# Performance work log

Measured on AMD Instinct MI355X. Metric: run time of the kernel, lower is better.

The kernel has to match this reference:

```python
import jax, jax.numpy as jnp
import numpy as np

B, L, D, N_LAYERS = 128, 256, 512, 6
NEG = -9e15  # -9000000000000000.0 in the torch source


def _pair_coef(a1, L, D):
    # Faithful reduction of the torch repeat_interleave(dim=2) construction:
    # first half of a_input satisfies a_input[b, i, j, m] = h[b, i, (j*D + m)//L],
    # so sum_m a_input[...,m]*a1[m] = h[b,i] . c[j] with
    # c[j, f] = sum_{m : (j*D+m)//L == f} a1[m].
    j = jnp.arange(L)[:, None]
    m = jnp.arange(D)[None, :]
    idx = (j * D + m) // L  # [L, D], values in [0, D-1]
    c = jnp.zeros((L, D), a1.dtype)
    c = c.at[jnp.arange(L)[:, None], idx].add(jnp.broadcast_to(a1[None, :], (L, D)))
    return c


def gat_layer(x, adj, W, a):
    # h = x @ W; e[b,i,j] = relu(a_input[b,i,j,:] @ a)  (relu overwrites leakyrelu in source)
    h = x @ W  # [B, L, D]
    d = W.shape[1]
    a1, a2 = a[:d, 0], a[d:, 0]
    c = _pair_coef(a1, h.shape[1], d)  # [L, D]
    e = jax.nn.relu(jnp.einsum('bif,jf->bij', h, c) + (h @ a2)[:, None, :])
    att = jnp.where(adj > 0, e, NEG)
    att = jax.nn.softmax(att, axis=2)  # dropout is identity in eval
    h_prime = jnp.einsum('bij,bjd->bid', att, h)
    return jax.nn.elu(h_prime)  # concat=True branch


def position_weight(x, left_len, aspect_len, text_len):
    j = jnp.arange(x.shape[1])[None, :].astype(jnp.float32)  # [1, L]
    l = left_len[:, None].astype(jnp.float32)
    r = (left_len + aspect_len - 1)[:, None].astype(jnp.float32)
    tl = text_len[:, None].astype(jnp.float32)
    ctx = (text_len - aspect_len)[:, None].astype(jnp.float32)
    w = jnp.where(j < l, 1.0 - (l - j) / ctx,
        jnp.where(j <= r, 0.0,
        jnp.where(j < tl, 1.0 - (j - r) / ctx, 0.0)))
    return w[..., None].astype(x.dtype) * x


def aspect_mask(x, left_len, aspect_len):
    j = jnp.arange(x.shape[1])[None, :]
    l = left_len[:, None]
    r = (left_len + aspect_len - 1)[:, None]
    m = ((j >= l) & (j <= r)).astype(x.dtype)
    return m[..., None] * x


def setup_inputs() -> dict:
    key = jax.random.key(0)
    ks = jax.random.split(key, 6)
    x = jax.random.normal(ks[0], (B, L, D), jnp.float32)
    adj = jax.random.randint(ks[1], (B, L, L), 0, 2, jnp.int32)
    adj = adj.at[:, jnp.arange(L), jnp.arange(L)].set(1)  # self loops
    left_len = jax.random.randint(ks[2], (B,), 0, 20, jnp.int32)
    aspect_len = jax.random.randint(ks[3], (B,), 1, 6, jnp.int32)
    text_len = jnp.full((B,), L, jnp.int32)
    W_stack = jax.random.normal(ks[4], (N_LAYERS, D, D), jnp.float32) * (1.414 / np.sqrt(D))
    a_stack = jax.random.normal(ks[5], (N_LAYERS, 2 * D, 1), jnp.float32) * 0.05
    return {"x": x, "W_stack": W_stack, "a_stack": a_stack, "adj": adj,
            "left_len": left_len, "aspect_len": aspect_len, "text_len": text_len}


def reference(x, W_stack, a_stack, adj, left_len, aspect_len, text_len):
    text_out = x
    xp = position_weight(text_out, left_len, aspect_len, text_len)
    h1 = jax.nn.relu(gat_layer(xp, adj, W_stack[0], a_stack[0]))
    h1 = position_weight(h1, left_len, aspect_len, text_len)
    x_graph = jnp.zeros_like(h1)
    for i in range(1, N_LAYERS):
        x_graph = x_graph + jax.nn.relu(gat_layer(h1, adj, W_stack[i], a_stack[i]))
    x_graph = 0.2 * x_graph
    graph_mask = aspect_mask(x_graph, left_len, aspect_len)
    # hop == 1 attention pooling
    alpha_mat = jnp.einsum('bld,bmd->blm', graph_mask, text_out)  # [B, L, L]
    alpha = jax.nn.softmax(alpha_mat.sum(axis=1, keepdims=True), axis=2)  # [B, 1, L]
    a1 = jnp.einsum('blm,bmd->bld', alpha, text_out)[:, 0, :]  # [B, D]
    return a1
```

## Files before the change

### kernel.cpp

```cpp
#include <hip/hip_runtime.h>

#define NB 128
#define NLQ 256
#define ND 512
#define NLAYERS 6
#define DD (ND*ND)
#define MN (1024*ND)
#define HTB 131072

typedef _Float16 f16x8 __attribute__((ext_vector_type(8)));
typedef __fp16 fp16x2 __attribute__((ext_vector_type(2)));
typedef _Float16 f16x4v __attribute__((ext_vector_type(4)));
typedef float f32x4 __attribute__((ext_vector_type(4)));
typedef unsigned int u32x2 __attribute__((ext_vector_type(2)));
typedef unsigned int u32x4 __attribute__((ext_vector_type(4)));
typedef unsigned short ushort_t;

#define GLOAD16(gp, lp) __builtin_amdgcn_global_load_lds( \
    (const __attribute__((address_space(1))) void*)(gp), \
    (__attribute__((address_space(3))) void*)(lp), 16, 0, 0)

__device__ __forceinline__ float wave_max(float v){
  #pragma unroll
  for(int off=32; off; off>>=1) v = fmaxf(v, __shfl_xor(v, off));
  return v;
}
__device__ __forceinline__ float wave_sum(float v){
  #pragma unroll
  for(int off=32; off; off>>=1) v += __shfl_xor(v, off);
  return v;
}
__device__ __forceinline__ unsigned int pk16(float a, float b){
  fp16x2 h = __builtin_amdgcn_cvt_pkrtz(a, b);
  return __builtin_bit_cast(unsigned int, h);
}

__global__ __launch_bounds__(256) void k_scal(const float* __restrict__ a_stack,
                                              float* __restrict__ scal){
  int layer = blockIdx.x;
  const float* a = a_stack + (size_t)layer*2*ND;
  int t = threadIdx.x;
  float v0 = a[t];
  float v1 = a[256 + t];
  v0 = wave_sum(v0); v1 = wave_sum(v1);
  __shared__ float s0[4], s1[4];
  int wave = t>>6, lane = t&63;
  if(lane==0){ s0[wave]=v0; s1[wave]=v1; }
  __syncthreads();
  if(t==0){
    scal[layer*2+0] = s0[0]+s0[1]+s0[2]+s0[3];
    scal[layer*2+1] = s1[0]+s1[1]+s1[2]+s1[3];
  }
}

__global__ __launch_bounds__(256) void k_wa2(const float* __restrict__ Wst,
                                             const float* __restrict__ ast,
                                             float* __restrict__ v){
  int l  = blockIdx.x >> 7;
  int rg = blockIdx.x & 127;
  int i  = rg*4 + (threadIdx.x>>6);
  int lane = threadIdx.x & 63;
  const float4* wr = (const float4*)(Wst + (size_t)(l+1)*DD + (size_t)i*ND);
  const float4* ar = (const float4*)(ast + (size_t)(l+1)*2*ND + ND);
  float4 w0=wr[lane], w1=wr[lane+64], a0=ar[lane], a1=ar[lane+64];
  float d = w0.x*a0.x + w0.y*a0.y + w0.z*a0.z + w0.w*a0.w
          + w1.x*a1.x + w1.y*a1.y + w1.z*a1.z + w1.w*a1.w;
  d = wave_sum(d);
  if(lane==0) v[l*ND + i] = d;
}

__global__ __launch_bounds__(256) void k_wcvt(const float* __restrict__ Wsrc,
                                              ushort_t* __restrict__ Ho){
  __shared__ float CT[64][65];
  int bid = blockIdx.x;
  int l  = bid >> 6;
  int kt = (bid >> 3) & 7, nt = bid & 7;
  const float* Wl = Wsrc + (size_t)l*DD;
  int t = threadIdx.x;
  int r = t >> 2, c4 = (t&3)*16;
  #pragma unroll
  for(int u=0;u<4;u++){
    float4 vv = *(const float4*)(Wl + (size_t)(kt*64+r)*ND + nt*64 + c4 + u*4);
    CT[r][c4+u*4+0]=vv.x; CT[r][c4+u*4+1]=vv.y;
    CT[r][c4+u*4+2]=vv.z; CT[r][c4+u*4+3]=vv.w;
  }
  __syncthreads();
  int n = t >> 2, kc = t & 3;
  unsigned int o[8];
  #pragma unroll
  for(int j=0;j<8;j++)
    o[j] = pk16(CT[kc*16 + 2*j][n], CT[kc*16 + 2*j + 1][n]);
  ushort_t* dh = Ho + (size_t)l*DD + (size_t)(nt*64+n)*ND + kt*64 + kc*16;
  *(u32x4*)(dh)     = (u32x4){o[0],o[1],o[2],o[3]};
  *(u32x4*)(dh + 8) = (u32x4){o[4],o[5],o[6],o[7]};
}

#define ROWB2 144
template<int MODE>
__device__ __forceinline__ void gemm_tile(const float* __restrict__ A,
                                          const ushort_t* __restrict__ Wth,
                                          float* __restrict__ C,
                                          unsigned int* __restrict__ hP,
                                          ushort_t* __restrict__ Pbuf,
                                          float* __restrict__ tp4,
                                          const float* __restrict__ a2,
                                          const float* __restrict__ scal,
                                          const int* __restrict__ left,
                                          const int* __restrict__ asp,
                                          const int* __restrict__ tl,
                                          int mtile, int ntile, unsigned char* lds){
  unsigned char* Ah = lds;
  unsigned char* Bh = lds + 128*ROWB2;

  int t = threadIdx.x;
  int m0 = mtile*128, n0 = ntile*128;
  int lane = t & 63, wid = t >> 6;
  int wr = wid >> 2, wcq = wid & 3;
  int lrow = lane & 15, kb = lane >> 4;

  f32x4 acc[4][2];
  #pragma unroll
  for(int mi=0;mi<4;mi++)
    #pragma unroll
    for(int ni=0;ni<2;ni++)
      acc[mi][ni] = (f32x4){0.f,0.f,0.f,0.f};

  int a_row = t >> 4;
  int a_sl  = t & 15;
  int w_n   = t >> 3;
  int w_sl  = t & 7;

  float wgt_[4] = {1.f,1.f,1.f,1.f};
  if(MODE == 1){
    int b = mtile >> 1;
    float lf=(float)left[b], aspf=(float)asp[b], tlf=(float)tl[b];
    float rr=lf+aspf-1.f, ctx=tlf-aspf;
    #pragma unroll
    for(int u=0;u<4;u++){
      float jf = (float)((mtile&1)*128 + a_row + u*32);
      float w;
      if(jf < lf)       w = 1.f-(lf-jf)/ctx;
      else if(jf <= rr) w = 0.f;
      else if(jf < tlf) w = 1.f-(jf-rr)/ctx;
      else              w = 0.f;
      wgt_[u] = w;
    }
  }

  float4 pa[4];
  u32x4 pwh[2];

  #pragma unroll
  for(int u=0;u<4;u++)
    pa[u] = *(const float4*)(A + (size_t)(m0 + a_row + u*32)*ND + a_sl*4);
  #pragma unroll
  for(int u=0;u<2;u++)
    pwh[u] = *(const u32x4*)(Wth + (size_t)(n0 + w_n + u*64)*ND + w_sl*8);

  for(int k0=0; k0<ND; k0+=64){
    #pragma unroll
    for(int u=0;u<4;u++){
      unsigned int c0 = pk16(pa[u].x*wgt_[u], pa[u].y*wgt_[u]);
      unsigned int c1 = pk16(pa[u].z*wgt_[u], pa[u].w*wgt_[u]);
      *(u32x2*)(Ah + (a_row + u*32)*ROWB2 + a_sl*8) = (u32x2){c0, c1};
    }
    #pragma unroll
    for(int u=0;u<2;u++)
      *(u32x4*)(Bh + (w_n + u*64)*ROWB2 + w_sl*16) = pwh[u];
    __syncthreads();

    if(k0 + 64 < ND){
      int kn = k0 + 64;
      #pragma unroll
      for(int u=0;u<4;u++)
        pa[u] = *(const float4*)(A + (size_t)(m0 + a_row + u*32)*ND + kn + a_sl*4);
      #pragma unroll
      for(int u=0;u<2;u++)
        pwh[u] = *(const u32x4*)(Wth + (size_t)(n0 + w_n + u*64)*ND + kn + w_sl*8);
    }

    #pragma unroll
    for(int ks=0; ks<2; ks++){
      f16x8 ah[4], bh[2];
      #pragma unroll
      for(int mi=0;mi<4;mi++)
        ah[mi] = *(const f16x8*)(Ah + (wr*64 + mi*16 + lrow)*ROWB2 + ks*64 + kb*16);
      #pragma unroll
      for(int ni=0;ni<2;ni++)
        bh[ni] = *(const f16x8*)(Bh + (wcq*32 + ni*16 + lrow)*ROWB2 + ks*64 + kb*16);
      #pragma unroll
      for(int mi=0;mi<4;mi++)
        #pragma unroll
        for(int ni=0;ni<2;ni++)
          acc[mi][ni] = __builtin_amdgcn_mfma_f32_16x16x32_f16(ah[mi], bh[ni], acc[mi][ni], 0,0,0);
    }
    __syncthreads();
  }

  int rg = lane >> 4;
  int cc = lane & 15;
  if(MODE == 0){
    #pragma unroll
    for(int mi=0;mi<4;mi++)
      #pragma unroll
      for(int ni=0;ni<2;ni++){
        int col = n0 + wcq*32 + ni*16 + cc;
        #pragma unroll
        for(int q=0;q<4;q++){
          int row = m0 + wr*64 + mi*16 + rg*4 + q;
          C[(size_t)row*ND + col] = acc[mi][ni][q];
        }
      }
  } else {
    float S0 = scal[0], S1 = scal[1];
    float* CT = (float*)lds;
    int b = m0 >> 8;
    int ibase = m0 & 255;
    int tr   = t >> 2;
    int tch  = t & 3;
    float tpsum = 0.f;
    #pragma unroll
    for(int p=0;p<2;p++){
      if((wcq>>1) == p){
        #pragma unroll
        for(int mi=0;mi<4;mi++)
          #pragma unroll
          for(int ni=0;ni<2;ni++)
            #pragma unroll
            for(int q=0;q<4;q++)
              CT[((wcq&1)*32 + ni*16 + cc)*130 + wr*64 + mi*16 + rg*4 + q] = acc[mi][ni][q];
      }
      __syncthreads();
      int lcol = t >> 6;
      int lrow2 = (t & 63)*2;
      #pragma unroll
      for(int u=0;u<8;u++){
        int c = lcol + u*8;
        float2 v2 = *(float2*)&CT[c*130 + lrow2];
        size_t uidx = ((size_t)b*HTB + (size_t)(n0 + p*64 + c)*256 + ibase + lrow2) >> 1;
        hP[uidx] = pk16(v2.x, v2.y);
      }
      {
        int cpr = t & 31;
        int rq  = t >> 5;
        #pragma unroll
        for(int rr2=0; rr2<8; rr2++){
          int row = rq*8 + rr2;
          float pval = S0*CT[(2*cpr)*130 + row] + S1*CT[(2*cpr+1)*130 + row];
          int ig = ibase + row;
          _Float16 ph = (_Float16)pval;
          size_t addr = (size_t)b*262144 + (size_t)(ig>>5)*32768
                      + (size_t)(ig&31)*256 + (n0>>1) + p*32 + cpr;
          Pbuf[addr] = __builtin_bit_cast(unsigned short, ph);
        }
      }
      #pragma unroll
      for(int cc2=0; cc2<16; cc2++){
        int c = tch*16 + cc2;
        tpsum = fmaf(CT[c*130 + tr], a2[n0 + p*64 + c], tpsum);
      }
      __syncthreads();
    }
    tpsum += __shfl_xor(tpsum, 1);
    tpsum += __shfl_xor(tpsum, 2);
    if(tch == 0) tp4[(n0>>7)*32768 + m0 + tr] = tpsum;
  }
}

__global__ __launch_bounds__(512) void k_gemm_t(const float* __restrict__ A,
                                                const ushort_t* __restrict__ Wth,
                                                unsigned int* __restrict__ hP,
                                                ushort_t* __restrict__ Pbuf,
                                                float* __restrict__ tp4,
                                                const float* __restrict__ a2,
                                                const float* __restrict__ scal,
                                                const int* __restrict__ left,
                                                const int* __restrict__ asp,
                                                const int* __restrict__ tl){
  __shared__ unsigned char lds[2*128*ROWB2];
  int bid = blockIdx.x;
  int ntile = (bid >> 3) & 3;
  int mtile = (bid & 7) | ((bid >> 5) << 3);
  gemm_tile<1>(A, Wth, nullptr, hP, Pbuf, tp4, a2, scal, left, asp, tl,
               mtile, ntile, lds);
}

__global__ __launch_bounds__(512) void k_gemm_b(const float* __restrict__ Abase, long aStride,
                                                const ushort_t* __restrict__ Wth,
                                                float* __restrict__ Cbase){
  __shared__ unsigned char lds[2*128*ROWB2];
  int l  = blockIdx.x >> 5;
  int tb = blockIdx.x & 31;
  gemm_tile<0>(Abase + (size_t)l*aStride, Wth + (size_t)l*DD,
               Cbase + (size_t)l*MN, nullptr, nullptr, nullptr,
               nullptr, nullptr, nullptr, nullptr, nullptr, tb>>2, tb&3, lds);
}

__global__ __launch_bounds__(256) void k_attn0(
    const ushort_t* __restrict__ hTH,
    const int* __restrict__ adj,
    const float* __restrict__ tpart,
    const int* __restrict__ left, const int* __restrict__ asp, const int* __restrict__ tl,
    float* __restrict__ PA){
  __shared__ unsigned char attH[32*512];
  __shared__ unsigned char BsH[16384];

  int bid = blockIdx.x;
  int b  = bid & 127;
  int ic = bid >> 7;
  int i0 = ic*32;
  int tid = threadIdx.x;
  int lane = tid & 63, w = tid >> 6;
  const ushort_t* HH = hTH + (size_t)b*HTB;
  const ushort_t* Pt = (const ushort_t*)PA + (size_t)b*262144 + (size_t)ic*32768;

  float t0v=0.f, t1v=0.f, t2v=0.f, t3v=0.f;
  #pragma unroll
  for(int nt=0; nt<4; nt++){
    float4 tv = ((const float4*)(tpart + nt*32768 + b*256))[lane];
    t0v += tv.x; t1v += tv.y; t2v += tv.z; t3v += tv.w;
  }

  for(int rr=0; rr<8; rr++){
    int il = w*8 + rr;
    int i  = i0 + il;
    f16x4v pv = *(const f16x4v*)(Pt + il*256 + lane*4);
    int4 av = ((const int4*)(adj + ((size_t)b*NLQ + i)*NLQ))[lane];
    float e0 = fmaxf((float)pv[0] + t0v, 0.f);
    float e1 = fmaxf((float)pv[1] + t1v, 0.f);
    float e2 = fmaxf((float)pv[2] + t2v, 0.f);
    float e3 = fmaxf((float)pv[3] + t3v, 0.f);
    float m = -3.0e38f;
    if(av.x>0) m = e0;
    if(av.y>0) m = fmaxf(m, e1);
    if(av.z>0) m = fmaxf(m, e2);
    if(av.w>0) m = fmaxf(m, e3);
    m = wave_max(m);
    float p0 = (av.x>0) ? __expf(e0-m) : 0.f;
    float p1 = (av.y>0) ? __expf(e1-m) : 0.f;
    float p2 = (av.z>0) ? __expf(e2-m) : 0.f;
    float p3 = (av.w>0) ? __expf(e3-m) : 0.f;
    float s = wave_sum(p0+p1+p2+p3);
    float inv = 1.f/s;
    unsigned int w0 = pk16(p0*inv, p1*inv);
    unsigned int w1 = pk16(p2*inv, p3*inv);
    int off = il*512 + ((lane*8) ^ ((il&7)<<4));
    *(u32x2*)(attH + off) = (u32x2){w0,w1};
  }

  int wm = w >> 1, wn = w & 1;
  int lrow = lane & 15, kb = lane >> 4;
  int rg = lane >> 4, cc = lane & 15;
  float lf=(float)left[b], aspf=(float)asp[b], tlf=(float)tl[b];
  float rrv=lf+aspf-1.f, ctx=tlf-aspf;
  int arow = wm*16 + lrow;
  int aswz = (arow&7)<<4;

  for(int dp=0; dp<2; dp++){
    int d0 = dp*256;
    f32x4 acc[8];
    #pragma unroll
    for(int ni=0;ni<8;ni++) acc[ni] = (f32x4){0.f,0.f,0.f,0.f};
    for(int ks=0; ks<8; ks++){
      int j0 = ks*32;
      __syncthreads();
      #pragma unroll
      for(int u=0;u<4;u++){
        int chunk = (u*4 + w)*64 + lane;
        int row = chunk >> 2, sl = chunk & 3;
        GLOAD16(HH + (size_t)(d0+row)*256 + j0 + sl*8, BsH + (u*4+w)*1024);
      }
      __syncthreads();
      int aoff = arow*512 + ((j0*2 + kb*16) ^ aswz);
      f16x8 ah = *(const f16x8*)(attH + aoff);
      #pragma unroll
      for(int ni=0; ni<8; ni++){
        f16x8 bh = *(const f16x8*)(BsH + (wn*128 + ni*16 + lrow)*64 + kb*16);
        acc[ni] = __builtin_amdgcn_mfma_f32_16x16x32_f16(ah, bh, acc[ni], 0,0,0);
      }
    }
    #pragma unroll
    for(int q=0;q<4;q++){
      int row = i0 + wm*16 + rg*4 + q;
      float fi = (float)row;
      float wgt;
      if(fi < lf)        wgt = 1.f-(lf-fi)/ctx;
      else if(fi <= rrv) wgt = 0.f;
      else if(fi < tlf)  wgt = 1.f-(fi-rrv)/ctx;
      else               wgt = 0.f;
      #pragma unroll
      for(int ni=0;ni<8;ni++){
        int col = d0 + wn*128 + ni*16 + cc;
        PA[((size_t)b*NLQ + row)*ND + col] = wgt*fmaxf(acc[ni][q], 0.f);
      }
    }
  }
}

__global__ __launch_bounds__(256) void k_tv(const float* __restrict__ h1,
                                            const float* __restrict__ v,
                                            float* __restrict__ T){
  int row  = blockIdx.x*4 + (threadIdx.x>>6);
  int lane = threadIdx.x & 63;
  const float4* hr = (const float4*)(h1 + (size_t)row*ND);
  float4 h0 = hr[lane], h1v = hr[lane+64];
  float s0,s1,s2,s3,s4;
  #define DOTV(SL, L) { \
    const float4* vr = (const float4*)(v + (L)*ND); \
    float4 v0 = vr[lane], v1 = vr[lane+64]; \
    float dd = h0.x*v0.x+h0.y*v0.y+h0.z*v0.z+h0.w*v0.w \
             + h1v.x*v1.x+h1v.y*v1.y+h1v.z*v1.z+h1v.w*v1.w; \
    SL = wave_sum(dd); }
  DOTV(s0,0) DOTV(s1,1) DOTV(s2,2) DOTV(s3,3) DOTV(s4,4)
  #undef DOTV
  if(lane==0){
    T[0*32768 + row]=s0; T[1*32768 + row]=s1; T[2*32768 + row]=s2;
    T[3*32768 + row]=s3; T[4*32768 + row]=s4;
  }
}

__global__ __launch_bounds__(256) void k_rows(const float* __restrict__ h1,
                                              const int* __restrict__ left, const int* __restrict__ asp,
                                              float* __restrict__ R){
  int b = blockIdx.x;
  int nk = asp[b], l0 = left[b];
  const float4* src = (const float4*)(h1 + (size_t)b*NLQ*ND);
  float4* dst = (float4*)(R + (size_t)b*8*ND);
  #pragma unroll
  for(int u=0; u<4; u++){
    int f4 = threadIdx.x + u*256;
    int k = f4 >> 7, c = f4 & 127;
    float4 val = (k<nk) ? src[(size_t)(l0+k)*128 + c] : (float4){0.f,0.f,0.f,0.f};
    dst[f4] = val;
  }
}

__global__ __launch_bounds__(256) void k_att5(const float* __restrict__ h1,
    const float* __restrict__ Hasp, const float* __restrict__ T,
    const int* __restrict__ adj, const float* __restrict__ scal,
    const int* __restrict__ left, const int* __restrict__ asp,
    float* __restrict__ y){
  __shared__ float att[5][260];
  int b  = blockIdx.x & 127;
  int l  = blockIdx.x >> 7;
  int tid = threadIdx.x, lane = tid&63, w = tid>>6;
  int nk = asp[b], l0 = left[b];
  float S0 = scal[2*(l+1)], S1 = scal[2*(l+1)+1];

  for(int k = w; k < 5; k += 4){
    if(k < nk){
      const float2* hrow = (const float2*)(Hasp + (size_t)l*MN + (size_t)(b*8+k)*ND);
      const int* arow = adj + ((size_t)b*NLQ + (l0+k))*NLQ;
      const float* Tl = T + l*32768 + b*256;
      float e[4]; int av[4];
      float m = -3.0e38f;
      #pragma unroll
      for(int q=0;q<4;q++){
        int j = lane + 64*q;
        float2 hp = hrow[j];
        av[q] = arow[j];
        e[q] = fmaxf(S0*hp.x + S1*hp.y + Tl[j], 0.f);
        if(av[q] > 0) m = fmaxf(m, e[q]);
      }
      m = wave_max(m);
      float pp[4]; float s = 0.f;
      #pragma unroll
      for(int q=0;q<4;q++){
        pp[q] = (av[q] > 0) ? __expf(e[q]-m) : 0.f;
        s += pp[q];
      }
      s = wave_sum(s);
      float inv = 1.f/s;
      #pragma unroll
      for(int q=0;q<4;q++) att[k][lane+64*q] = pp[q]*inv;
    } else {
      #pragma unroll
      for(int q=0;q<4;q++) att[k][lane+64*q] = 0.f;
    }
  }
  __syncthreads();

  int d = tid;
  const float* hb = h1 + (size_t)b*NLQ*ND;
  float ax[5] = {0,0,0,0,0}, ay[5] = {0,0,0,0,0};
  for(int jj=0; jj<NLQ; jj++){
    float hx = hb[(size_t)jj*ND + d];
    float hy = hb[(size_t)jj*ND + 256 + d];
    #pragma unroll
    for(int k=0;k<5;k++){
      float a = att[k][jj];
      ax[k] += a*hx;
      ay[k] += a*hy;
    }
  }
  float* yb = y + (size_t)l*MN + (size_t)b*8*ND;
  #pragma unroll
  for(int k=0;k<5;k++){
    yb[(size_t)k*ND + d]       = ax[k];
    yb[(size_t)k*ND + 256 + d] = ay[k];
  }
  #pragma unroll
  for(int u=0;u<6;u++) yb[5*ND + u*256 + tid] = 0.f;
}

__global__ __launch_bounds__(256) void k_g(const float* __restrict__ hp,
    const int* __restrict__ asp, float* __restrict__ g){
  int b = blockIdx.x, d = threadIdx.x;
  int nk = asp[b];
  float gx=0.f, gy=0.f;
  for(int l=0;l<5;l++){
    for(int k=0;k<nk;k++){
      const float* r = hp + (size_t)l*MN + (size_t)(b*8+k)*ND;
      gx += fmaxf(r[d], 0.f);
      gy += fmaxf(r[d+256], 0.f);
    }
  }
  g[b*ND + d]       = 0.2f*gx;
  g[b*ND + 256 + d] = 0.2f*gy;
}

__global__ __launch_bounds__(256) void k_dot(const float* __restrict__ x,
    const float* __restrict__ g, float* __restrict__ s){
  int row  = blockIdx.x*4 + (threadIdx.x>>6);
  int b    = row >> 8;
  int lane = threadIdx.x & 63;
  const float4* xr = (const float4*)(x + (size_t)row*ND);
  const float4* gr = (const float4*)(g + (size_t)b*ND);
  float4 x0=xr[lane], x1=xr[lane+64], g0=gr[lane], g1=gr[lane+64];
  float d = x0.x*g0.x + x0.y*g0.y + x0.z*g0.z + x0.w*g0.w
          + x1.x*g1.x + x1.y*g1.y + x1.z*g1.z + x1.w*g1.w;
  d = wave_sum(d);
  if(lane==0) s[row] = d;
}

__global__ __launch_bounds__(256) void k_out(const float* __restrict__ x,
    const float* __restrict__ s, float* __restrict__ out){
  int b  = blockIdx.x >> 2;
  int ch = blockIdx.x & 3;
  int tid = threadIdx.x, lane = tid&63, w = tid>>6;
  __shared__ float red[4];
  __shared__ float alpha[NLQ];
  __shared__ float part[128];
  float sv = s[b*NLQ + tid];
  float m = wave_max(sv);
  if(lane==0) red[w] = m;
  __syncthreads();
  m = fmaxf(fmaxf(red[0],red[1]), fmaxf(red[2],red[3]));
  float p = __expf(sv - m);
  float su = wave_sum(p);
  __syncthreads();
  if(lane==0) red[w] = su;
  __syncthreads();
  su = red[0]+red[1]+red[2]+red[3];
  alpha[tid] = p/su;
  __syncthreads();
  int d = ch*128 + (tid & 127);
  int half = tid >> 7;
  const float* xb = x + (size_t)b*NLQ*ND;
  float acc = 0.f;
  for(int mm = half*128; mm < half*128 + 128; mm++)
    acc += alpha[mm] * xb[(size_t)mm*ND + d];
  if(half) part[tid & 127] = acc;
  __syncthreads();
  if(!half) out[(size_t)b*ND + d] = acc + part[tid & 127];
}

extern "C" void kernel_launch(void* const* d_in, const int* in_sizes, int n_in,
                              void* d_out, int out_size, void* d_ws, size_t ws_size,
                              hipStream_t stream){
  const float* x    = (const float*)d_in[0];
  const float* Wst  = (const float*)d_in[1];
  const float* ast  = (const float*)d_in[2];
  const int*   adj  = (const int*)d_in[3];
  const int*   left = (const int*)d_in[4];
  const int*   asp  = (const int*)d_in[5];
  const int*   tl   = (const int*)d_in[6];
  float* out = (float*)d_out;
  float* ws  = (float*)d_ws;

  const size_t SZ = (size_t)NB*NLQ*ND;
  float* bufA = ws;
  float* bufB = ws + SZ;
  float* ws2  = ws + 2*SZ;
  float* tpart= ws2;
  float* T    = tpart + 4*32768;
  float* g    = T + 163840;
  float* scal = g + 65536;
  float* v    = scal + 16;
  float* sbuf = v + 2560;
  ushort_t* w0th = (ushort_t*)(sbuf + 32768);

  ushort_t* hTH = (ushort_t*)bufB;

  float* Hasp = bufB;
  float* ybuf = Hasp + (size_t)5*MN;
  float* hp   = ybuf + (size_t)5*MN;
  float* R    = hp   + (size_t)5*MN;
  ushort_t* wt15h = (ushort_t*)(R + MN);

  k_scal<<<NLAYERS, 256, 0, stream>>>(ast, scal);
  k_wa2<<<5*128, 256, 0, stream>>>(Wst, ast, v);
  k_wcvt<<<64, 256, 0, stream>>>(Wst, w0th);

  k_gemm_t<<<(NB*NLQ/128)*(ND/128), 512, 0, stream>>>(x, w0th,
      (unsigned int*)hTH, (ushort_t*)bufA, tpart, ast + ND, scal, left, asp, tl);
  k_attn0<<<NB*8, 256, 0, stream>>>(hTH, adj, tpart, left, asp, tl, bufA);

  k_wcvt<<<5*64, 256, 0, stream>>>(Wst + DD, wt15h);
  k_tv<<<NB*NLQ/4, 256, 0, stream>>>(bufA, v, T);
  k_rows<<<NB, 256, 0, stream>>>(bufA, left, asp, R);
  k_gemm_b<<<5*32, 512, 0, stream>>>(R, 0L, wt15h, Hasp);
  k_att5<<<5*NB, 256, 0, stream>>>(bufA, Hasp, T, adj, scal, left, asp, ybuf);
  k_gemm_b<<<5*32, 512, 0, stream>>>(ybuf, (long)MN, wt15h, hp);
  k_g<<<NB, 256, 0, stream>>>(hp, asp, g);

  k_dot<<<NB*NLQ/4, 256, 0, stream>>>(x, g, sbuf);
  k_out<<<NB*4, 256, 0, stream>>>(x, sbuf, out);
}
```

Before: 208.6 us.

## Pre-convert GEMM A operands to fp16 and double-buffer via direct global-to-LDS loads

Adds a pre-pass kernel that applies the position weight and converts x to fp16. The GEMM producers (k_rows, k_att5) now also emit fp16 operands. The GEMM tile loop drops its register-staged fp32-to-fp16 conversion and instead uses global_load_lds into a double-buffered 64KB LDS with an unpadded 128-byte row stride, overlapping the next K-slice load with the MFMAs. The cost is an extra launch and a full write plus read of the fp16 copy of x. The larger LDS footprint reduces occupancy, and the unpadded rows may cause LDS bank conflicts.

```diff
diff --git a/kernel.cpp b/kernel.cpp
--- a/kernel.cpp
+++ b/kernel.cpp
@@ -95,9 +95,30 @@
   *(u32x4*)(dh + 8) = (u32x4){o[4],o[5],o[6],o[7]};
 }
 
-#define ROWB2 144
+__global__ __launch_bounds__(256) void k_xposw(const float* __restrict__ x,
+    ushort_t* __restrict__ xp,
+    const int* __restrict__ left, const int* __restrict__ asp, const int* __restrict__ tl){
+  int c = blockIdx.x*256 + threadIdx.x;
+  int row = c >> 6;
+  int b = row >> 8;
+  float jf = (float)(row & 255);
+  float lf=(float)left[b], aspf=(float)asp[b], tlf=(float)tl[b];
+  float rr=lf+aspf-1.f, ctx=tlf-aspf;
+  float w;
+  if(jf < lf)       w = 1.f-(lf-jf)/ctx;
+  else if(jf <= rr) w = 0.f;
+  else if(jf < tlf) w = 1.f-(jf-rr)/ctx;
+  else              w = 0.f;
+  const float4* xr = (const float4*)x;
+  float4 v0 = xr[(size_t)c*2], v1 = xr[(size_t)c*2+1];
+  u32x4 o = (u32x4){ pk16(v0.x*w, v0.y*w), pk16(v0.z*w, v0.w*w),
+                     pk16(v1.x*w, v1.y*w), pk16(v1.z*w, v1.w*w) };
+  *(u32x4*)(xp + (size_t)c*8) = o;
+}
+
+#define BKB 128
 template<int MODE>
-__device__ __forceinline__ void gemm_tile(const float* __restrict__ A,
+__device__ __forceinline__ void gemm_tile(const ushort_t* __restrict__ A16,
                                           const ushort_t* __restrict__ Wth,
                                           float* __restrict__ C,
                                           unsigned int* __restrict__ hP,
@@ -105,13 +126,7 @@
                                           float* __restrict__ tp4,
                                           const float* __restrict__ a2,
                                           const float* __restrict__ scal,
-                                          const int* __restrict__ left,
-                                          const int* __restrict__ asp,
-                                          const int* __restrict__ tl,
                                           int mtile, int ntile, unsigned char* lds){
-  unsigned char* Ah = lds;
-  unsigned char* Bh = lds + 128*ROWB2;
-
   int t = threadIdx.x;
   int m0 = mtile*128, n0 = ntile*128;
   int lane = t & 63, wid = t >> 6;
@@ -125,69 +140,42 @@
     for(int ni=0;ni<2;ni++)
       acc[mi][ni] = (f32x4){0.f,0.f,0.f,0.f};
 
-  int a_row = t >> 4;
-  int a_sl  = t & 15;
-  int w_n   = t >> 3;
-  int w_sl  = t & 7;
-
-  float wgt_[4] = {1.f,1.f,1.f,1.f};
-  if(MODE == 1){
-    int b = mtile >> 1;
-    float lf=(float)left[b], aspf=(float)asp[b], tlf=(float)tl[b];
-    float rr=lf+aspf-1.f, ctx=tlf-aspf;
-    #pragma unroll
-    for(int u=0;u<4;u++){
-      float jf = (float)((mtile&1)*128 + a_row + u*32);
-      float w;
-      if(jf < lf)       w = 1.f-(lf-jf)/ctx;
-      else if(jf <= rr) w = 0.f;
-      else if(jf < tlf) w = 1.f-(jf-rr)/ctx;
-      else              w = 0.f;
-      wgt_[u] = w;
-    }
-  }
-
-  float4 pa[4];
-  u32x4 pwh[2];
-
-  #pragma unroll
-  for(int u=0;u<4;u++)
-    pa[u] = *(const float4*)(A + (size_t)(m0 + a_row + u*32)*ND + a_sl*4);
-  #pragma unroll
-  for(int u=0;u<2;u++)
-    pwh[u] = *(const u32x4*)(Wth + (size_t)(n0 + w_n + u*64)*ND + w_sl*8);
-
-  for(int k0=0; k0<ND; k0+=64){
-    #pragma unroll
-    for(int u=0;u<4;u++){
-      unsigned int c0 = pk16(pa[u].x*wgt_[u], pa[u].y*wgt_[u]);
-      unsigned int c1 = pk16(pa[u].z*wgt_[u], pa[u].w*wgt_[u]);
-      *(u32x2*)(Ah + (a_row + u*32)*ROWB2 + a_sl*8) = (u32x2){c0, c1};
-    }
-    #pragma unroll
-    for(int u=0;u<2;u++)
-      *(u32x4*)(Bh + (w_n + u*64)*ROWB2 + w_sl*16) = pwh[u];
-    __syncthreads();
-
-    if(k0 + 64 < ND){
-      int kn = k0 + 64;
-      #pragma unroll
-      for(int u=0;u<4;u++)
-        pa[u] = *(const float4*)(A + (size_t)(m0 + a_row + u*32)*ND + kn + a_sl*4);
-      #pragma unroll
-      for(int u=0;u<2;u++)
-        pwh[u] = *(const u32x4*)(Wth + (size_t)(n0 + w_n + u*64)*ND + kn + w_sl*8);
-    }
-
+  int s_row = t >> 3;
+  int s_sl  = t & 7;
+  int dstoff = wid*1024;
+
+  const ushort_t* Asrc0 = A16 + (size_t)(m0 + s_row)*ND + s_sl*8;
+  const ushort_t* Asrc1 = A16 + (size_t)(m0 + 64 + s_row)*ND + s_sl*8;
+  const ushort_t* Bsrc0 = Wth + (size_t)(n0 + s_row)*ND + s_sl*8;
+  const ushort_t* Bsrc1 = Wth + (size_t)(n0 + 64 + s_row)*ND + s_sl*8;
+
+  GLOAD16(Asrc0, lds + dstoff);
+  GLOAD16(Asrc1, lds + 8192 + dstoff);
+  GLOAD16(Bsrc0, lds + 16384 + dstoff);
+  GLOAD16(Bsrc1, lds + 24576 + dstoff);
+  __syncthreads();
+
+  int cur = 0;
+  for(int it=0; it<8; ++it){
+    if(it < 7){
+      int kn = (it+1)*64;
+      unsigned char* dst = lds + ((cur^1)<<15);
+      GLOAD16(Asrc0 + kn, dst + dstoff);
+      GLOAD16(Asrc1 + kn, dst + 8192 + dstoff);
+      GLOAD16(Bsrc0 + kn, dst + 16384 + dstoff);
+      GLOAD16(Bsrc1 + kn, dst + 24576 + dstoff);
+    }
+    unsigned char* Ab = lds + (cur<<15);
+    unsigned char* Bb = Ab + 16384;
     #pragma unroll
     for(int ks=0; ks<2; ks++){
       f16x8 ah[4], bh[2];
       #pragma unroll
       for(int mi=0;mi<4;mi++)
-        ah[mi] = *(const f16x8*)(Ah + (wr*64 + mi*16 + lrow)*ROWB2 + ks*64 + kb*16);
+        ah[mi] = *(const f16x8*)(Ab + (wr*64 + mi*16 + lrow)*BKB + ks*64 + kb*16);
       #pragma unroll
       for(int ni=0;ni<2;ni++)
-        bh[ni] = *(const f16x8*)(Bh + (wcq*32 + ni*16 + lrow)*ROWB2 + ks*64 + kb*16);
+        bh[ni] = *(const f16x8*)(Bb + (wcq*32 + ni*16 + lrow)*BKB + ks*64 + kb*16);
       #pragma unroll
       for(int mi=0;mi<4;mi++)
         #pragma unroll
@@ -195,6 +183,7 @@
           acc[mi][ni] = __builtin_amdgcn_mfma_f32_16x16x32_f16(ah[mi], bh[ni], acc[mi][ni], 0,0,0);
     }
     __syncthreads();
+    cur ^= 1;
   }
 
   int rg = lane >> 4;
@@ -267,33 +256,29 @@
   }
 }
 
-__global__ __launch_bounds__(512) void k_gemm_t(const float* __restrict__ A,
+__global__ __launch_bounds__(512) void k_gemm_t(const ushort_t* __restrict__ A16,
                                                 const ushort_t* __restrict__ Wth,
                                                 unsigned int* __restrict__ hP,
                                                 ushort_t* __restrict__ Pbuf,
                                                 float* __restrict__ tp4,
                                                 const float* __restrict__ a2,
-                                                const float* __restrict__ scal,
-                                                const int* __restrict__ left,
-                                                const int* __restrict__ asp,
-                                                const int* __restrict__ tl){
-  __shared__ unsigned char lds[2*128*ROWB2];
+                                                const float* __restrict__ scal){
+  __shared__ unsigned char lds[65536];
   int bid = blockIdx.x;
   int ntile = (bid >> 3) & 3;
   int mtile = (bid & 7) | ((bid >> 5) << 3);
-  gemm_tile<1>(A, Wth, nullptr, hP, Pbuf, tp4, a2, scal, left, asp, tl,
-               mtile, ntile, lds);
-}
-
-__global__ __launch_bounds__(512) void k_gemm_b(const float* __restrict__ Abase, long aStride,
+  gemm_tile<1>(A16, Wth, nullptr, hP, Pbuf, tp4, a2, scal, mtile, ntile, lds);
+}
+
+__global__ __launch_bounds__(512) void k_gemm_b(const ushort_t* __restrict__ Abase, long aStride,
                                                 const ushort_t* __restrict__ Wth,
                                                 float* __restrict__ Cbase){
-  __shared__ unsigned char lds[2*128*ROWB2];
+  __shared__ unsigned char lds[65536];
   int l  = blockIdx.x >> 5;
   int tb = blockIdx.x & 31;
   gemm_tile<0>(Abase + (size_t)l*aStride, Wth + (size_t)l*DD,
                Cbase + (size_t)l*MN, nullptr, nullptr, nullptr,
-               nullptr, nullptr, nullptr, nullptr, nullptr, tb>>2, tb&3, lds);
+               nullptr, nullptr, tb>>2, tb&3, lds);
 }
 
 __global__ __launch_bounds__(256) void k_attn0(
@@ -421,17 +406,17 @@
 
 __global__ __launch_bounds__(256) void k_rows(const float* __restrict__ h1,
                                               const int* __restrict__ left, const int* __restrict__ asp,
-                                              float* __restrict__ R){
+                                              ushort_t* __restrict__ R){
   int b = blockIdx.x;
   int nk = asp[b], l0 = left[b];
-  const float4* src = (const float4*)(h1 + (size_t)b*NLQ*ND);
-  float4* dst = (float4*)(R + (size_t)b*8*ND);
-  #pragma unroll
-  for(int u=0; u<4; u++){
-    int f4 = threadIdx.x + u*256;
-    int k = f4 >> 7, c = f4 & 127;
-    float4 val = (k<nk) ? src[(size_t)(l0+k)*128 + c] : (float4){0.f,0.f,0.f,0.f};
-    dst[f4] = val;
+  const float* src = h1 + (size_t)b*NLQ*ND;
+  unsigned int* dst = (unsigned int*)(R + (size_t)b*8*ND);
+  #pragma unroll
+  for(int u=0; u<8; u++){
+    int idx = threadIdx.x + u*256;
+    int k = idx >> 8, c = idx & 255;
+    float2 vv = (k<nk) ? ((const float2*)(src + (size_t)(l0+k)*ND))[c] : (float2){0.f,0.f};
+    dst[idx] = pk16(vv.x, vv.y);
   }
 }
 
@@ -439,7 +424,7 @@
     const float* __restrict__ Hasp, const float* __restrict__ T,
     const int* __restrict__ adj, const float* __restrict__ scal,
     const int* __restrict__ left, const int* __restrict__ asp,
-    float* __restrict__ y){
+    ushort_t* __restrict__ y){
   __shared__ float att[5][260];
   int b  = blockIdx.x & 127;
   int l  = blockIdx.x >> 7;
@@ -493,14 +478,14 @@
       ay[k] += a*hy;
     }
   }
-  float* yb = y + (size_t)l*MN + (size_t)b*8*ND;
+  ushort_t* yb = y + (size_t)l*MN + (size_t)b*8*ND;
   #pragma unroll
   for(int k=0;k<5;k++){
-    yb[(size_t)k*ND + d]       = ax[k];
-    yb[(size_t)k*ND + 256 + d] = ay[k];
-  }
-  #pragma unroll
-  for(int u=0;u<6;u++) yb[5*ND + u*256 + tid] = 0.f;
+    yb[(size_t)k*ND + d]       = __builtin_bit_cast(unsigned short, (_Float16)ax[k]);
+    yb[(size_t)k*ND + 256 + d] = __builtin_bit_cast(unsigned short, (_Float16)ay[k]);
+  }
+  #pragma unroll
+  for(int u=0;u<6;u++) yb[5*ND + u*256 + tid] = 0;
 }
 
 __global__ __launch_bounds__(256) void k_g(const float* __restrict__ hp,
@@ -590,28 +575,30 @@
   float* sbuf = v + 2560;
   ushort_t* w0th = (ushort_t*)(sbuf + 32768);
 
-  ushort_t* hTH = (ushort_t*)bufB;
+  ushort_t* hTH  = (ushort_t*)bufB;
+  ushort_t* xp16 = (ushort_t*)(bufB + (SZ>>1));
 
   float* Hasp = bufB;
-  float* ybuf = Hasp + (size_t)5*MN;
-  float* hp   = ybuf + (size_t)5*MN;
-  float* R    = hp   + (size_t)5*MN;
-  ushort_t* wt15h = (ushort_t*)(R + MN);
+  ushort_t* y16 = (ushort_t*)(Hasp + (size_t)5*MN);
+  float* hp   = Hasp + (size_t)10*MN;
+  ushort_t* R16 = (ushort_t*)(hp + (size_t)5*MN);
+  ushort_t* wt15h = (ushort_t*)(hp + (size_t)5*MN + (MN>>1));
 
   k_scal<<<NLAYERS, 256, 0, stream>>>(ast, scal);
   k_wa2<<<5*128, 256, 0, stream>>>(Wst, ast, v);
   k_wcvt<<<64, 256, 0, stream>>>(Wst, w0th);
-
-  k_gemm_t<<<(NB*NLQ/128)*(ND/128), 512, 0, stream>>>(x, w0th,
-      (unsigned int*)hTH, (ushort_t*)bufA, tpart, ast + ND, scal, left, asp, tl);
+  k_xposw<<<8192, 256, 0, stream>>>(x, xp16, left, asp, tl);
+
+  k_gemm_t<<<(NB*NLQ/128)*(ND/128), 512, 0, stream>>>(xp16, w0th,
+      (unsigned int*)hTH, (ushort_t*)bufA, tpart, ast + ND, scal);
   k_attn0<<<NB*8, 256, 0, stream>>>(hTH, adj, tpart, left, asp, tl, bufA);
 
   k_wcvt<<<5*64, 256, 0, stream>>>(Wst + DD, wt15h);
   k_tv<<<NB*NLQ/4, 256, 0, stream>>>(bufA, v, T);
-  k_rows<<<NB, 256, 0, stream>>>(bufA, left, asp, R);
-  k_gemm_b<<<5*32, 512, 0, stream>>>(R, 0L, wt15h, Hasp);
-  k_att5<<<5*NB, 256, 0, stream>>>(bufA, Hasp, T, adj, scal, left, asp, ybuf);
-  k_gemm_b<<<5*32, 512, 0, stream>>>(ybuf, (long)MN, wt15h, hp);
+  k_rows<<<NB, 256, 0, stream>>>(bufA, left, asp, R16);
+  k_gemm_b<<<5*32, 512, 0, stream>>>(R16, 0L, wt15h, Hasp);
+  k_att5<<<5*NB, 256, 0, stream>>>(bufA, Hasp, T, adj, scal, left, asp, y16);
+  k_gemm_b<<<5*32, 512, 0, stream>>>(y16, (long)MN, wt15h, hp);
   k_g<<<NB, 256, 0, stream>>>(hp, asp, g);
 
   k_dot<<<NB*NLQ/4, 256, 0, stream>>>(x, g, sbuf);
```

After: 225.0 us. 1.08x slower.
